# Kernel tuning notes

Hardware: AMD Instinct MI355X
Metric: run time of the kernel (lower is better)

Reference implementation:

```python
import jax, jax.numpy as jnp
import numpy as np

N = 262144        # number of nodes
D = 64            # fixed in-degree per destination node (edges grouped by dest)
RATIO = 0.5
K = int(D * RATIO)  # edges kept per node = 32


def setup_inputs() -> dict:
    key = jax.random.key(0)
    k1, k2 = jax.random.split(key)
    logits = jax.random.normal(k1, (N,), dtype=jnp.float32)
    # source endpoints: random nodes; destination endpoints: sorted, D edges per node
    src = jax.random.randint(k2, (N * D,), 0, N, dtype=jnp.int32)
    dst = jnp.repeat(jnp.arange(N, dtype=jnp.int32), D)
    edge_index = jnp.stack([src, dst])  # [2, E]
    return {"logits": logits, "edge_index": edge_index}


def reference(logits, edge_index):
    # LabelAwarePool.forward: sigmoid -> per-edge L1 similarity -> per-dest-node top-k edges
    s = jax.nn.sigmoid(logits).reshape(-1)          # [N]
    ends = s[edge_index]                            # [2, E] endpoint scores
    sim = 1.0 - jnp.abs(ends[0] - ends[1])          # [E] similarity
    E = edge_index.shape[1]
    n = E // D                                      # number of segments (nodes)
    # segmented top-k: edges are grouped by destination node in blocks of D
    _, idx = jax.lax.top_k(sim.reshape(n, D), K)    # [n, K] indices within each segment
    edges_g = edge_index.reshape(2, n, D)           # [2, n, D]
    sel = jnp.take_along_axis(edges_g, idx[None, :, :], axis=2)  # [2, n, K]
    return sel.reshape(2, n * K)                    # concatenated kept edges
```

## Files before the change

kernel.cpp:

```cpp
#include <hip/hip_runtime.h>
#include <cstdint>

#define D_EDGES 64
#define K_KEEP  32

__device__ __forceinline__ float np_expf(float x) {
    const float log2e     = 1.44269504088896341f;
    const float cvt_magic = 12582912.0f;
    const float neg_ln2hi = -0.693359375f;
    const float neg_ln2lo = 2.12194440e-4f;
    const float p0 = 1.9875691500E-4f;
    const float p1 = 1.3981999507E-3f;
    const float p2 = 8.3334519073E-3f;
    const float p3 = 4.1665795894E-2f;
    const float p4 = 1.6666665459E-1f;
    const float p5 = 5.0000001201E-1f;

    float q = fmaf(x, log2e, cvt_magic);
    q -= cvt_magic;
    x = fmaf(q, neg_ln2hi, x);
    x = fmaf(q, neg_ln2lo, x);
    float x2 = x * x;
    float poly = fmaf(p0, x, p1);
    poly = fmaf(poly, x, p2);
    poly = fmaf(poly, x, p3);
    poly = fmaf(poly, x, p4);
    poly = fmaf(poly, x, p5);
    poly = fmaf(poly, x2, x);
    poly = poly + 1.0f;
    return ldexpf(poly, (int)q);
}

__device__ __forceinline__ float sigmoid_np(float x) {
    float e = np_expf(-x);
    return 1.0f / (1.0f + e);
}

__global__ void sigmoid_kernel(const float* __restrict__ logits,
                               float* __restrict__ s, int n) {
    int i = blockIdx.x * blockDim.x + threadIdx.x;
    if (i < n) s[i] = sigmoid_np(logits[i]);
}

template <int CTRL>
__device__ __forceinline__ unsigned xor_dpp_u32(unsigned v) {
    return (unsigned)__builtin_amdgcn_update_dpp((int)v, (int)v, CTRL, 0xF, 0xF, true);
}

template <int J>
__device__ __forceinline__ unsigned xorshfl_u32(unsigned v, int addr32) {
    if constexpr (J == 1)       return xor_dpp_u32<0xB1>(v);
    else if constexpr (J == 2)  return xor_dpp_u32<0x4E>(v);
    else if constexpr (J == 4)  return (unsigned)__builtin_amdgcn_ds_swizzle((int)v, 0x101F);
    else if constexpr (J == 8)  return xor_dpp_u32<0x128>(v);
    else if constexpr (J == 16) return (unsigned)__builtin_amdgcn_ds_swizzle((int)v, 0x401F);
    else                        return (unsigned)__builtin_amdgcn_ds_bpermute(addr32, (int)v);
}

template <int J>
__device__ __forceinline__ void stage32(unsigned& key, bool dir, int addr32) {
    unsigned other = xorshfl_u32<J>(key, addr32);
    unsigned mx = (key > other) ? key : other;
    unsigned mn = (key > other) ? other : key;
    key = dir ? mx : mn;
}

template <int CTRL>
__device__ __forceinline__ unsigned long long xor_dpp_u64(unsigned long long v) {
    int lo = (int)(unsigned)v;
    int hi = (int)(v >> 32);
    lo = __builtin_amdgcn_update_dpp(lo, lo, CTRL, 0xF, 0xF, true);
    hi = __builtin_amdgcn_update_dpp(hi, hi, CTRL, 0xF, 0xF, true);
    return ((unsigned long long)(unsigned)hi << 32) | (unsigned)lo;
}

template <int OFF>
__device__ __forceinline__ unsigned long long xor_swz_u64(unsigned long long v) {
    int lo = (int)(unsigned)v;
    int hi = (int)(v >> 32);
    lo = __builtin_amdgcn_ds_swizzle(lo, OFF);
    hi = __builtin_amdgcn_ds_swizzle(hi, OFF);
    return ((unsigned long long)(unsigned)hi << 32) | (unsigned)lo;
}

template <int J>
__device__ __forceinline__ unsigned long long xorshfl_u64(unsigned long long v) {
    if constexpr (J == 1)       return xor_dpp_u64<0xB1>(v);
    else if constexpr (J == 2)  return xor_dpp_u64<0x4E>(v);
    else if constexpr (J == 4)  return xor_swz_u64<0x101F>(v);
    else if constexpr (J == 8)  return xor_dpp_u64<0x128>(v);
    else if constexpr (J == 16) return xor_swz_u64<0x401F>(v);
    else {
        int lo = (int)(unsigned)v;
        int hi = (int)(v >> 32);
        lo = __shfl_xor(lo, 32, 64);
        hi = __shfl_xor(hi, 32, 64);
        return ((unsigned long long)(unsigned)hi << 32) | (unsigned)lo;
    }
}

template <int K, int J>
__device__ __forceinline__ void stage64(unsigned long long& key, int lane) {
    unsigned long long other = xorshfl_u64<J>(key);
    const bool dir = ((lane & J) == 0) == ((lane & K) == 0);
    key = ((key > other) != dir) ? other : key;
}

__global__ __launch_bounds__(256)
void topk_kernel(const int* __restrict__ edge_index,
                 const float* __restrict__ stab,
                 int* __restrict__ out,
                 int E, int nseg, int outHalf) {
    const int tid = threadIdx.x;
    const int lane = tid & 63;
    const int w = (blockIdx.x << 2) | (tid >> 6);
    if (w >= nseg) return;
    const int e = (w << 6) | lane;

    int src = edge_index[e];
    int dst = edge_index[E + e];

    float ss = stab[src];
    float sd = stab[__builtin_amdgcn_readfirstlane(dst)];
    float sim = 1.0f - fabsf(ss - sd);

    const bool b1  = (lane & 1)  == 0;
    const bool b2  = (lane & 2)  == 0;
    const bool b4  = (lane & 4)  == 0;
    const bool b8  = (lane & 8)  == 0;
    const bool b16 = (lane & 16) == 0;
    const bool b32 = (lane & 32) == 0;
    const int addr32 = (lane ^ 32) << 2;

    int origLane;
    if (__all(sim >= 0.0625f)) {
        unsigned kb = __float_as_uint(sim);
        unsigned key = ((kb - 0x3D800000u) << 6) | (unsigned)(lane ^ 63);

        stage32<1>(key, b1 == b2, addr32);
        stage32<2>(key, b2 == b4, addr32);  stage32<1>(key, b1 == b4, addr32);
        stage32<4>(key, b4 == b8, addr32);  stage32<2>(key, b2 == b8, addr32);
        stage32<1>(key, b1 == b8, addr32);
        stage32<8>(key, b8 == b16, addr32); stage32<4>(key, b4 == b16, addr32);
        stage32<2>(key, b2 == b16, addr32); stage32<1>(key, b1 == b16, addr32);
        stage32<16>(key, b16 == b32, addr32); stage32<8>(key, b8 == b32, addr32);
        stage32<4>(key, b4 == b32, addr32);   stage32<2>(key, b2 == b32, addr32);
        stage32<1>(key, b1 == b32, addr32);
        stage32<32>(key, b32, addr32); stage32<16>(key, b16, addr32);
        stage32<8>(key, b8, addr32);   stage32<4>(key, b4, addr32);
        stage32<2>(key, b2, addr32);   stage32<1>(key, b1, addr32);

        origLane = ((int)key & 63) ^ 63;
    } else {
        unsigned long long key =
            ((unsigned long long)__float_as_uint(sim) << 6) |
            (unsigned long long)(lane ^ 63);
        stage64<2, 1>(key, lane);
        stage64<4, 2>(key, lane);   stage64<4, 1>(key, lane);
        stage64<8, 4>(key, lane);   stage64<8, 2>(key, lane);   stage64<8, 1>(key, lane);
        stage64<16, 8>(key, lane);  stage64<16, 4>(key, lane);  stage64<16, 2>(key, lane);
        stage64<16, 1>(key, lane);
        stage64<32, 16>(key, lane); stage64<32, 8>(key, lane);  stage64<32, 4>(key, lane);
        stage64<32, 2>(key, lane);  stage64<32, 1>(key, lane);
        stage64<64, 32>(key, lane); stage64<64, 16>(key, lane); stage64<64, 8>(key, lane);
        stage64<64, 4>(key, lane);  stage64<64, 2>(key, lane);  stage64<64, 1>(key, lane);
        origLane = ((int)(key & 63)) ^ 63;
    }

    int sel_src = __builtin_amdgcn_ds_bpermute(origLane << 2, src);

    int col = lane & 31;
    int base = (w << 5) | col;
    bool hiHalf = lane >= 32;
    out[hiHalf ? (outHalf + base) : base] = hiHalf ? dst : sel_src;
}

extern "C" void kernel_launch(void* const* d_in, const int* in_sizes, int n_in,
                              void* d_out, int out_size, void* d_ws, size_t ws_size,
                              hipStream_t stream) {
    const float* logits = (const float*)d_in[0];
    const int* edge_index = (const int*)d_in[1];
    int N = in_sizes[0];
    int E = in_sizes[1] / 2;
    int nseg = E / D_EDGES;
    int outHalf = nseg * K_KEEP;
    int* out = (int*)d_out;

    float* stab = (float*)d_ws;
    sigmoid_kernel<<<(N + 255) / 256, 256, 0, stream>>>(logits, stab, N);

    int blocks = (nseg + 3) / 4;
    topk_kernel<<<blocks, 256, 0, stream>>>(edge_index, stab, out,
                                            E, nseg, outHalf);
}
```

Baseline: 283.4 us.

## Process two segments per wavefront with interleaved bitonic sorts

```diff
diff --git a/kernel.cpp b/kernel.cpp
--- a/kernel.cpp
+++ b/kernel.cpp
@@ -58,11 +58,16 @@
 }
 
 template <int J>
-__device__ __forceinline__ void stage32(unsigned& key, bool dir, int addr32) {
-    unsigned other = xorshfl_u32<J>(key, addr32);
-    unsigned mx = (key > other) ? key : other;
-    unsigned mn = (key > other) ? other : key;
-    key = dir ? mx : mn;
+__device__ __forceinline__ void stage32x2(unsigned& ka, unsigned& kb,
+                                          bool dir, int addr32) {
+    unsigned oa = xorshfl_u32<J>(ka, addr32);
+    unsigned ob = xorshfl_u32<J>(kb, addr32);
+    unsigned mxa = (ka > oa) ? ka : oa;
+    unsigned mna = (ka > oa) ? oa : ka;
+    unsigned mxb = (kb > ob) ? kb : ob;
+    unsigned mnb = (kb > ob) ? ob : kb;
+    ka = dir ? mxa : mna;
+    kb = dir ? mxb : mnb;
 }
 
 template <int CTRL>
@@ -106,6 +111,22 @@
     key = ((key > other) != dir) ? other : key;
 }
 
+__device__ __noinline__ int sort64_slow(float sim, int lane) {
+    unsigned long long key =
+        ((unsigned long long)__float_as_uint(sim) << 6) |
+        (unsigned long long)(lane ^ 63);
+    stage64<2, 1>(key, lane);
+    stage64<4, 2>(key, lane);   stage64<4, 1>(key, lane);
+    stage64<8, 4>(key, lane);   stage64<8, 2>(key, lane);   stage64<8, 1>(key, lane);
+    stage64<16, 8>(key, lane);  stage64<16, 4>(key, lane);  stage64<16, 2>(key, lane);
+    stage64<16, 1>(key, lane);
+    stage64<32, 16>(key, lane); stage64<32, 8>(key, lane);  stage64<32, 4>(key, lane);
+    stage64<32, 2>(key, lane);  stage64<32, 1>(key, lane);
+    stage64<64, 32>(key, lane); stage64<64, 16>(key, lane); stage64<64, 8>(key, lane);
+    stage64<64, 4>(key, lane);  stage64<64, 2>(key, lane);  stage64<64, 1>(key, lane);
+    return ((int)(key & 63)) ^ 63;
+}
+
 __global__ __launch_bounds__(256)
 void topk_kernel(const int* __restrict__ edge_index,
                  const float* __restrict__ stab,
@@ -113,16 +134,26 @@
                  int E, int nseg, int outHalf) {
     const int tid = threadIdx.x;
     const int lane = tid & 63;
-    const int w = (blockIdx.x << 2) | (tid >> 6);
-    if (w >= nseg) return;
-    const int e = (w << 6) | lane;
-
-    int src = edge_index[e];
-    int dst = edge_index[E + e];
-
-    float ss = stab[src];
-    float sd = stab[__builtin_amdgcn_readfirstlane(dst)];
-    float sim = 1.0f - fabsf(ss - sd);
+    const int wp = (blockIdx.x << 2) | (tid >> 6);
+    const int segA = wp << 1;
+    if (segA >= nseg) return;
+    const int segB = segA + 1;
+    const bool hasB = segB < nseg;
+
+    const int baseA = segA << 6;
+    int srcA = edge_index[baseA + lane];
+    int srcB = hasB ? edge_index[baseA + 64 + lane] : 0;
+
+    int sbase = __builtin_amdgcn_readfirstlane(baseA);
+    int dstA = edge_index[E + sbase];
+    int dstB = hasB ? edge_index[E + sbase + 64] : dstA;
+
+    float sdA = stab[dstA];
+    float sdB = stab[dstB];
+    float ssA = stab[srcA];
+    float ssB = stab[srcB];
+    float simA = 1.0f - fabsf(ssA - sdA);
+    float simB = hasB ? (1.0f - fabsf(ssB - sdB)) : 1.0f;
 
     const bool b1  = (lane & 1)  == 0;
     const bool b2  = (lane & 2)  == 0;
@@ -132,47 +163,43 @@
     const bool b32 = (lane & 32) == 0;
     const int addr32 = (lane ^ 32) << 2;
 
-    int origLane;
-    if (__all(sim >= 0.0625f)) {
-        unsigned kb = __float_as_uint(sim);
-        unsigned key = ((kb - 0x3D800000u) << 6) | (unsigned)(lane ^ 63);
-
-        stage32<1>(key, b1 == b2, addr32);
-        stage32<2>(key, b2 == b4, addr32);  stage32<1>(key, b1 == b4, addr32);
-        stage32<4>(key, b4 == b8, addr32);  stage32<2>(key, b2 == b8, addr32);
-        stage32<1>(key, b1 == b8, addr32);
-        stage32<8>(key, b8 == b16, addr32); stage32<4>(key, b4 == b16, addr32);
-        stage32<2>(key, b2 == b16, addr32); stage32<1>(key, b1 == b16, addr32);
-        stage32<16>(key, b16 == b32, addr32); stage32<8>(key, b8 == b32, addr32);
-        stage32<4>(key, b4 == b32, addr32);   stage32<2>(key, b2 == b32, addr32);
-        stage32<1>(key, b1 == b32, addr32);
-        stage32<32>(key, b32, addr32); stage32<16>(key, b16, addr32);
-        stage32<8>(key, b8, addr32);   stage32<4>(key, b4, addr32);
-        stage32<2>(key, b2, addr32);   stage32<1>(key, b1, addr32);
-
-        origLane = ((int)key & 63) ^ 63;
+    int origA, origB;
+    if (__all(fminf(simA, simB) >= 0.0625f)) {
+        unsigned ka = ((__float_as_uint(simA) - 0x3D800000u) << 6) | (unsigned)(lane ^ 63);
+        unsigned kb = ((__float_as_uint(simB) - 0x3D800000u) << 6) | (unsigned)(lane ^ 63);
+
+        stage32x2<1>(ka, kb, b1 == b2, addr32);
+        stage32x2<2>(ka, kb, b2 == b4, addr32);  stage32x2<1>(ka, kb, b1 == b4, addr32);
+        stage32x2<4>(ka, kb, b4 == b8, addr32);  stage32x2<2>(ka, kb, b2 == b8, addr32);
+        stage32x2<1>(ka, kb, b1 == b8, addr32);
+        stage32x2<8>(ka, kb, b8 == b16, addr32); stage32x2<4>(ka, kb, b4 == b16, addr32);
+        stage32x2<2>(ka, kb, b2 == b16, addr32); stage32x2<1>(ka, kb, b1 == b16, addr32);
+        stage32x2<16>(ka, kb, b16 == b32, addr32); stage32x2<8>(ka, kb, b8 == b32, addr32);
+        stage32x2<4>(ka, kb, b4 == b32, addr32);   stage32x2<2>(ka, kb, b2 == b32, addr32);
+        stage32x2<1>(ka, kb, b1 == b32, addr32);
+        stage32x2<32>(ka, kb, b32, addr32); stage32x2<16>(ka, kb, b16, addr32);
+        stage32x2<8>(ka, kb, b8, addr32);   stage32x2<4>(ka, kb, b4, addr32);
+        stage32x2<2>(ka, kb, b2, addr32);   stage32x2<1>(ka, kb, b1, addr32);
+
+        origA = ((int)ka & 63) ^ 63;
+        origB = ((int)kb & 63) ^ 63;
     } else {
-        unsigned long long key =
-            ((unsigned long long)__float_as_uint(sim) << 6) |
-            (unsigned long long)(lane ^ 63);
-        stage64<2, 1>(key, lane);
-        stage64<4, 2>(key, lane);   stage64<4, 1>(key, lane);
-        stage64<8, 4>(key, lane);   stage64<8, 2>(key, lane);   stage64<8, 1>(key, lane);
-        stage64<16, 8>(key, lane);  stage64<16, 4>(key, lane);  stage64<16, 2>(key, lane);
-        stage64<16, 1>(key, lane);
-        stage64<32, 16>(key, lane); stage64<32, 8>(key, lane);  stage64<32, 4>(key, lane);
-        stage64<32, 2>(key, lane);  stage64<32, 1>(key, lane);
-        stage64<64, 32>(key, lane); stage64<64, 16>(key, lane); stage64<64, 8>(key, lane);
-        stage64<64, 4>(key, lane);  stage64<64, 2>(key, lane);  stage64<64, 1>(key, lane);
-        origLane = ((int)(key & 63)) ^ 63;
-    }
-
-    int sel_src = __builtin_amdgcn_ds_bpermute(origLane << 2, src);
-
-    int col = lane & 31;
-    int base = (w << 5) | col;
-    bool hiHalf = lane >= 32;
-    out[hiHalf ? (outHalf + base) : base] = hiHalf ? dst : sel_src;
+        origA = sort64_slow(simA, lane);
+        origB = sort64_slow(simB, lane);
+    }
+
+    int selA = __builtin_amdgcn_ds_bpermute(origA << 2, srcA);
+    int selB = __builtin_amdgcn_ds_bpermute(origB << 2, srcB);
+
+    if (lane < K_KEEP) {
+        int base = (segA << 5) | lane;
+        out[base] = selA;
+        if (hasB) out[base + K_KEEP] = selB;
+    }
+    if (lane < K_KEEP || hasB) {
+        int dstv = (lane < K_KEEP) ? dstA : dstB;
+        out[outHalf + (segA << 5) + lane] = dstv;
+    }
 }
 
 extern "C" void kernel_launch(void* const* d_in, const int* in_sizes, int n_in,
@@ -189,7 +216,8 @@
     float* stab = (float*)d_ws;
     sigmoid_kernel<<<(N + 255) / 256, 256, 0, stream>>>(logits, stab, N);
 
-    int blocks = (nseg + 3) / 4;
+    int npairs = (nseg + 1) / 2;
+    int blocks = (npairs + 3) / 4;
     topk_kernel<<<blocks, 256, 0, stream>>>(edge_index, stab, out,
                                             E, nseg, outHalf);
 }
```

Measured after the change: 293.0 us. 3.4% more time.
